# Performance work log

Measured on AMD Instinct MI355X. Metric: run time of the kernel, lower is better.

## Reference

```python
import jax, jax.numpy as jnp
import numpy as np

NEG = -1e6  # mask value used by d2l-style masked_softmax


def masked_softmax(scores, valid_lens):
    # scores: [B, Q, K]; valid_lens: [B] int — mask key positions j >= valid_len
    K = scores.shape[-1]
    mask = jnp.arange(K, dtype=jnp.int32)[None, None, :] < valid_lens[:, None, None]
    scores = jnp.where(mask, scores, NEG)
    return jax.nn.softmax(scores, axis=-1)


def setup_inputs() -> dict:
    key = jax.random.key(0)
    kq, kk, kv, kl = jax.random.split(key, 4)
    B, Q, K, d = 16, 4096, 4096, 128
    queries = jax.random.normal(kq, (B, Q, d), dtype=jnp.float32)
    keys = jax.random.normal(kk, (B, K, d), dtype=jnp.float32)
    values = jax.random.normal(kv, (B, K, d), dtype=jnp.float32)
    valid_lens = jax.random.randint(kl, (B,), 1, K + 1, dtype=jnp.int32)
    return {"queries": queries, "keys": keys, "values": values,
            "valid_lens": valid_lens}


def reference(queries, keys, values, valid_lens):
    d = queries.shape[-1]
    # [B, Q, K] scores = Q K^T / sqrt(d)
    scores = jnp.einsum('bqd,bkd->bqk', queries, keys) / jnp.sqrt(
        jnp.asarray(d, queries.dtype))
    attn = masked_softmax(scores, valid_lens)
    # dropout is identity in eval mode
    return jnp.einsum('bqk,bkd->bqd', attn, values)
```

## Files before the change

kernel.cpp:

```cpp
#include <hip/hip_runtime.h>
#include <stdint.h>

typedef __attribute__((ext_vector_type(8))) short short8;
typedef __attribute__((ext_vector_type(4))) float float4v;
typedef __attribute__((ext_vector_type(16))) float f32x16;

#define B_  16
#define S_  4096
#define D_  128
#define TM  64
#define TN  64
#define NT_ (S_ / TN)
#define IMG 8192

#define ZERO16 {0.f,0.f,0.f,0.f, 0.f,0.f,0.f,0.f, 0.f,0.f,0.f,0.f, 0.f,0.f,0.f,0.f}

__device__ __forceinline__ unsigned short f2bf(float f) {
    union { float f; uint32_t u; } c; c.f = f;
    uint32_t u = c.u + 0x7FFFu + ((c.u >> 16) & 1u);
    return (unsigned short)(u >> 16);
}

__device__ __forceinline__ uint4 pack8(float4v x, float4v y) {
    uint4 r;
    r.x = (uint32_t)f2bf(x[0]) | ((uint32_t)f2bf(x[1]) << 16);
    r.y = (uint32_t)f2bf(x[2]) | ((uint32_t)f2bf(x[3]) << 16);
    r.z = (uint32_t)f2bf(y[0]) | ((uint32_t)f2bf(y[1]) << 16);
    r.w = (uint32_t)f2bf(y[2]) | ((uint32_t)f2bf(y[3]) << 16);
    return r;
}

__device__ __forceinline__ void gload16(const unsigned short* g, unsigned short* l) {
    __builtin_amdgcn_global_load_lds(
        (const __attribute__((address_space(1))) unsigned int*)g,
        (__attribute__((address_space(3))) unsigned int*)l, 16, 0, 0);
}

__device__ __forceinline__ uint32_t cvtpk(float lo, float hi) {
    uint32_t w;
    asm("v_cvt_pk_bf16_f32 %0, %1, %2" : "=v"(w) : "v"(lo), "v"(hi));
    return w;
}

__device__ __forceinline__ short8 build_pfrag(const float* p) {
    uint32_t xa = cvtpk(p[0], p[1]);
    uint32_t xb = cvtpk(p[2], p[3]);
    uint32_t ya = cvtpk(p[4], p[5]);
    uint32_t yb = cvtpk(p[6], p[7]);
    asm("v_permlane32_swap_b32 %0, %1" : "+v"(xa), "+v"(ya));
    asm("v_permlane32_swap_b32 %0, %1" : "+v"(xb), "+v"(yb));
    union { uint32_t u[4]; short8 s; } r;
    r.u[0] = xa; r.u[1] = xb; r.u[2] = ya; r.u[3] = yb;
    return r.s;
}

__global__ __launch_bounds__(256)
void prepass(const float* __restrict__ Kg, const float* __restrict__ Vg,
             unsigned short* __restrict__ Kb, unsigned short* __restrict__ Vb)
{
    const int t = threadIdx.x;
    const int tile = blockIdx.x, b = blockIdx.y;
    const size_t img = (size_t)(b * NT_ + tile) * IMG;

    const float* ksrc = Kg + ((size_t)b * S_ + tile * TN) * D_;
    const float* vsrc = Vg + ((size_t)b * S_ + tile * TN) * D_;
    unsigned short* kdst = Kb + img;
    unsigned short* vdst = Vb + img;

    float4v kx[4], ky[4];
    #pragma unroll
    for (int i = 0; i < 4; ++i) {
        int bid = i * 256 + t;
        int row = bid >> 4, cbp = bid & 15;
        int cb  = cbp ^ (row & 15);
        const float* s = ksrc + row * D_ + cb * 8;
        kx[i] = *(const float4v*)s;
        ky[i] = *(const float4v*)(s + 4);
    }
    const int kb = t >> 5, cg = t & 31;
    float4v v[8];
    #pragma unroll
    for (int r = 0; r < 8; ++r)
        v[r] = *(const float4v*)(vsrc + (kb * 8 + r) * D_ + cg * 4);

    #pragma unroll
    for (int i = 0; i < 4; ++i) {
        int bid = i * 256 + t;
        *(uint4*)(kdst + (size_t)bid * 8) = pack8(kx[i], ky[i]);
    }

    #pragma unroll
    for (int j = 0; j < 4; ++j) {
        int dr = cg * 4 + j;
        uint4 w;
        w.x = (uint32_t)f2bf(v[0][j]) | ((uint32_t)f2bf(v[1][j]) << 16);
        w.y = (uint32_t)f2bf(v[2][j]) | ((uint32_t)f2bf(v[3][j]) << 16);
        w.z = (uint32_t)f2bf(v[4][j]) | ((uint32_t)f2bf(v[5][j]) << 16);
        w.w = (uint32_t)f2bf(v[6][j]) | ((uint32_t)f2bf(v[7][j]) << 16);
        *(uint4*)(vdst + dr * 64 + (kb ^ (dr & 7)) * 8) = w;
    }
}

__global__ __launch_bounds__(128, 2)
void attn_fwd(const float* __restrict__ Qg,
              const unsigned short* __restrict__ Kb,
              const unsigned short* __restrict__ Vb,
              const int* __restrict__ VL,
              float* __restrict__ Og)
{
    __shared__ __align__(16) unsigned short Ks[TN * D_];
    __shared__ __align__(16) unsigned short Vt[D_ * TN];

    const int t    = threadIdx.x;
    const int wave = t >> 6;
    const int lane = t & 63;
    const int l31  = lane & 31;
    const int hi   = lane >> 5;

    const int b  = blockIdx.y;
    const int q0 = blockIdx.x * TM;
    const int nvalid = VL[b];
    const int ntiles = (nvalid + TN - 1) / TN;

    const float qscale = 0.08838834764831845f * 1.4426950408889634f;

    short8 qf[8];
    {
        const float* qp = Qg + ((size_t)b * S_ + (q0 + wave * 32 + l31)) * D_;
        #pragma unroll
        for (int ks = 0; ks < 8; ++ks) {
            float4v x = *(const float4v*)(qp + ks * 16 + hi * 8);
            float4v y = *(const float4v*)(qp + ks * 16 + hi * 8 + 4);
            #pragma unroll
            for (int j = 0; j < 4; ++j) { x[j] *= qscale; y[j] *= qscale; }
            union { uint4 u; short8 s; } cv; cv.u = pack8(x, y);
            qf[ks] = cv.s;
        }
    }

    f32x16 zz = ZERO16;
    f32x16 oacc[4];
    oacc[0] = zz; oacc[1] = zz; oacc[2] = zz; oacc[3] = zz;
    float lsum = 0.f;

    const int swk = l31 & 15;
    const int swv = l31 & 7;

    for (int tile = 0; tile < ntiles; ++tile) {
        const int n0 = tile * TN;
        __syncthreads();

        {
            const unsigned short* kimg = Kb + (size_t)(b * NT_ + tile) * IMG;
            const unsigned short* vimg = Vb + (size_t)(b * NT_ + tile) * IMG;
            #pragma unroll
            for (int i = 0; i < 8; ++i) {
                int go = (i * 128 + t) * 8;
                int lo = (i * 128 + wave * 64) * 8;
                gload16(kimg + go, &Ks[lo]);
                gload16(vimg + go, &Vt[lo]);
            }
        }
        __syncthreads();

        f32x16 st0 = zz, st1 = zz;
        {
            const unsigned short* k0 = &Ks[l31 * D_];
            const unsigned short* k1 = &Ks[(32 + l31) * D_];
            __builtin_amdgcn_s_setprio(1);
            #pragma unroll
            for (int ks = 0; ks < 8; ++ks) {
                int sl = (((ks << 1) | hi) ^ swk) << 3;
                short8 a0 = *(const short8*)(k0 + sl);
                short8 a1 = *(const short8*)(k1 + sl);
                st0 = __builtin_amdgcn_mfma_f32_32x32x16_bf16(a0, qf[ks], st0, 0, 0, 0);
                st1 = __builtin_amdgcn_mfma_f32_32x32x16_bf16(a1, qf[ks], st1, 0, 0, 0);
            }
            __builtin_amdgcn_s_setprio(0);
        }

        float p0[16], p1[16];
        const bool full = (n0 + TN) <= nvalid;
        if (full) {
            #pragma unroll
            for (int r = 0; r < 16; ++r) { p0[r] = exp2f(st0[r]); lsum += p0[r]; }
            #pragma unroll
            for (int r = 0; r < 16; ++r) { p1[r] = exp2f(st1[r]); lsum += p1[r]; }
        } else {
            #pragma unroll
            for (int r = 0; r < 16; ++r) {
                int key = n0 + (r & 3) + 8 * (r >> 2) + 4 * hi;
                float e = exp2f(st0[r]);
                p0[r] = (key < nvalid) ? e : 0.f; lsum += p0[r];
            }
            #pragma unroll
            for (int r = 0; r < 16; ++r) {
                int key = n0 + 32 + (r & 3) + 8 * (r >> 2) + 4 * hi;
                float e = exp2f(st1[r]);
                p1[r] = (key < nvalid) ? e : 0.f; lsum += p1[r];
            }
        }

        short8 pf0 = build_pfrag(p0);
        short8 pf1 = build_pfrag(p0 + 8);
        short8 pf2 = build_pfrag(p1);
        short8 pf3 = build_pfrag(p1 + 8);

        __builtin_amdgcn_s_setprio(1);
        #pragma unroll
        for (int dt = 0; dt < 4; ++dt) {
            const unsigned short* vrow = &Vt[(dt * 32 + l31) * TN];
            short8 v0 = *(const short8*)(vrow + ((((0 << 1) | hi) ^ swv) << 3));
            short8 v1 = *(const short8*)(vrow + ((((1 << 1) | hi) ^ swv) << 3));
            short8 v2 = *(const short8*)(vrow + ((((2 << 1) | hi) ^ swv) << 3));
            short8 v3 = *(const short8*)(vrow + ((((3 << 1) | hi) ^ swv) << 3));
            oacc[dt] = __builtin_amdgcn_mfma_f32_32x32x16_bf16(pf0, v0, oacc[dt], 0, 0, 0);
            oacc[dt] = __builtin_amdgcn_mfma_f32_32x32x16_bf16(pf1, v1, oacc[dt], 0, 0, 0);
            oacc[dt] = __builtin_amdgcn_mfma_f32_32x32x16_bf16(pf2, v2, oacc[dt], 0, 0, 0);
            oacc[dt] = __builtin_amdgcn_mfma_f32_32x32x16_bf16(pf3, v3, oacc[dt], 0, 0, 0);
        }
        __builtin_amdgcn_s_setprio(0);
    }

    float ltot = lsum + __shfl_xor(lsum, 32);
    float inv  = 1.0f / ltot;

    float* op = Og + ((size_t)b * S_ + (q0 + wave * 32)) * D_ + l31;
    #pragma unroll
    for (int r = 0; r < 16; ++r) {
        const int qc = (r & 3) + 8 * (r >> 2);
        float invr = __shfl(inv, qc + 4 * hi, 32);
        #pragma unroll
        for (int dt = 0; dt < 4; ++dt)
            op[(qc + 4 * hi) * D_ + dt * 32] = oacc[dt][r] * invr;
    }
}

extern "C" void kernel_launch(void* const* d_in, const int* in_sizes, int n_in,
                              void* d_out, int out_size, void* d_ws, size_t ws_size,
                              hipStream_t stream) {
    const float* Q = (const float*)d_in[0];
    const float* K = (const float*)d_in[1];
    const float* V = (const float*)d_in[2];
    const int*   L = (const int*)d_in[3];
    float*       O = (float*)d_out;

    unsigned short* Kb = (unsigned short*)d_ws;
    unsigned short* Vb = Kb + (size_t)B_ * S_ * D_;

    dim3 grid(NT_, B_);
    prepass<<<grid, 256, 0, stream>>>(K, V, Kb, Vb);
    dim3 grid2(S_ / TM, B_);
    attn_fwd<<<grid2, 128, 0, stream>>>(Q, Kb, Vb, L, O);
}
```

Baseline: 240.2 us.

## Split key tile across two wave pairs and reduce partial outputs in shared memory

Doubles the block to four waves. Each pair of waves still covers the same 32 query rows, but each wave handles only half of the 64 keys in a tile, so per-wave MFMA work and register pressure are halved. Partial output accumulators and row sums from the second key half are reduced through shared memory at the end. The aim is more waves in flight to hide latency, at the cost of an extra LDS reduction, more barriers, and an occupancy target of four blocks in launch bounds.

```diff
diff --git a/kernel.cpp b/kernel.cpp
--- a/kernel.cpp
+++ b/kernel.cpp
@@ -101,21 +101,25 @@
     }
 }
 
-__global__ __launch_bounds__(128, 2)
+__global__ __launch_bounds__(256, 4)
 void attn_fwd(const float* __restrict__ Qg,
               const unsigned short* __restrict__ Kb,
               const unsigned short* __restrict__ Vb,
               const int* __restrict__ VL,
               float* __restrict__ Og)
 {
-    __shared__ __align__(16) unsigned short Ks[TN * D_];
-    __shared__ __align__(16) unsigned short Vt[D_ * TN];
+    __shared__ __align__(16) unsigned short SM[2 * IMG];
+    __shared__ float Ls[128];
+    unsigned short* Ks = SM;
+    unsigned short* Vt = SM + IMG;
 
     const int t    = threadIdx.x;
     const int wave = t >> 6;
     const int lane = t & 63;
     const int l31  = lane & 31;
     const int hi   = lane >> 5;
+    const int wq   = wave >> 1;
+    const int wk   = wave & 1;
 
     const int b  = blockIdx.y;
     const int q0 = blockIdx.x * TM;
@@ -126,7 +130,7 @@
 
     short8 qf[8];
     {
-        const float* qp = Qg + ((size_t)b * S_ + (q0 + wave * 32 + l31)) * D_;
+        const float* qp = Qg + ((size_t)b * S_ + (q0 + wq * 32 + l31)) * D_;
         #pragma unroll
         for (int ks = 0; ks < 8; ++ks) {
             float4v x = *(const float4v*)(qp + ks * 16 + hi * 8);
@@ -154,85 +158,91 @@
             const unsigned short* kimg = Kb + (size_t)(b * NT_ + tile) * IMG;
             const unsigned short* vimg = Vb + (size_t)(b * NT_ + tile) * IMG;
             #pragma unroll
-            for (int i = 0; i < 8; ++i) {
-                int go = (i * 128 + t) * 8;
-                int lo = (i * 128 + wave * 64) * 8;
+            for (int i = 0; i < 4; ++i) {
+                int go = (i * 256 + t) * 8;
+                int lo = (i * 256 + wave * 64) * 8;
                 gload16(kimg + go, &Ks[lo]);
                 gload16(vimg + go, &Vt[lo]);
             }
         }
         __syncthreads();
 
-        f32x16 st0 = zz, st1 = zz;
+        f32x16 st = zz;
         {
-            const unsigned short* k0 = &Ks[l31 * D_];
-            const unsigned short* k1 = &Ks[(32 + l31) * D_];
+            const unsigned short* k0 = &Ks[(wk * 32 + l31) * D_];
             __builtin_amdgcn_s_setprio(1);
             #pragma unroll
             for (int ks = 0; ks < 8; ++ks) {
                 int sl = (((ks << 1) | hi) ^ swk) << 3;
                 short8 a0 = *(const short8*)(k0 + sl);
-                short8 a1 = *(const short8*)(k1 + sl);
-                st0 = __builtin_amdgcn_mfma_f32_32x32x16_bf16(a0, qf[ks], st0, 0, 0, 0);
-                st1 = __builtin_amdgcn_mfma_f32_32x32x16_bf16(a1, qf[ks], st1, 0, 0, 0);
+                st = __builtin_amdgcn_mfma_f32_32x32x16_bf16(a0, qf[ks], st, 0, 0, 0);
             }
             __builtin_amdgcn_s_setprio(0);
         }
 
-        float p0[16], p1[16];
+        float p[16];
         const bool full = (n0 + TN) <= nvalid;
         if (full) {
             #pragma unroll
-            for (int r = 0; r < 16; ++r) { p0[r] = exp2f(st0[r]); lsum += p0[r]; }
-            #pragma unroll
-            for (int r = 0; r < 16; ++r) { p1[r] = exp2f(st1[r]); lsum += p1[r]; }
+            for (int r = 0; r < 16; ++r) { p[r] = exp2f(st[r]); lsum += p[r]; }
         } else {
             #pragma unroll
             for (int r = 0; r < 16; ++r) {
-                int key = n0 + (r & 3) + 8 * (r >> 2) + 4 * hi;
-                float e = exp2f(st0[r]);
-                p0[r] = (key < nvalid) ? e : 0.f; lsum += p0[r];
+                int key = n0 + wk * 32 + (r & 3) + 8 * (r >> 2) + 4 * hi;
+                float e = exp2f(st[r]);
+                p[r] = (key < nvalid) ? e : 0.f; lsum += p[r];
             }
-            #pragma unroll
-            for (int r = 0; r < 16; ++r) {
-                int key = n0 + 32 + (r & 3) + 8 * (r >> 2) + 4 * hi;
-                float e = exp2f(st1[r]);
-                p1[r] = (key < nvalid) ? e : 0.f; lsum += p1[r];
-            }
-        }
-
-        short8 pf0 = build_pfrag(p0);
-        short8 pf1 = build_pfrag(p0 + 8);
-        short8 pf2 = build_pfrag(p1);
-        short8 pf3 = build_pfrag(p1 + 8);
+        }
+
+        short8 pf0 = build_pfrag(p);
+        short8 pf1 = build_pfrag(p + 8);
 
         __builtin_amdgcn_s_setprio(1);
         #pragma unroll
         for (int dt = 0; dt < 4; ++dt) {
             const unsigned short* vrow = &Vt[(dt * 32 + l31) * TN];
-            short8 v0 = *(const short8*)(vrow + ((((0 << 1) | hi) ^ swv) << 3));
-            short8 v1 = *(const short8*)(vrow + ((((1 << 1) | hi) ^ swv) << 3));
-            short8 v2 = *(const short8*)(vrow + ((((2 << 1) | hi) ^ swv) << 3));
-            short8 v3 = *(const short8*)(vrow + ((((3 << 1) | hi) ^ swv) << 3));
+            int s0 = ((((wk * 2 + 0) << 1) | hi) ^ swv) << 3;
+            int s1 = ((((wk * 2 + 1) << 1) | hi) ^ swv) << 3;
+            short8 v0 = *(const short8*)(vrow + s0);
+            short8 v1 = *(const short8*)(vrow + s1);
             oacc[dt] = __builtin_amdgcn_mfma_f32_32x32x16_bf16(pf0, v0, oacc[dt], 0, 0, 0);
             oacc[dt] = __builtin_amdgcn_mfma_f32_32x32x16_bf16(pf1, v1, oacc[dt], 0, 0, 0);
-            oacc[dt] = __builtin_amdgcn_mfma_f32_32x32x16_bf16(pf2, v2, oacc[dt], 0, 0, 0);
-            oacc[dt] = __builtin_amdgcn_mfma_f32_32x32x16_bf16(pf3, v3, oacc[dt], 0, 0, 0);
         }
         __builtin_amdgcn_s_setprio(0);
     }
 
-    float ltot = lsum + __shfl_xor(lsum, 32);
-    float inv  = 1.0f / ltot;
-
-    float* op = Og + ((size_t)b * S_ + (q0 + wave * 32)) * D_ + l31;
-    #pragma unroll
-    for (int r = 0; r < 16; ++r) {
-        const int qc = (r & 3) + 8 * (r >> 2);
-        float invr = __shfl(inv, qc + 4 * hi, 32);
+    float lpart = lsum + __shfl_xor(lsum, 32);
+
+    float* red = (float*)SM;
+    __syncthreads();
+    if (wk == 1) {
         #pragma unroll
         for (int dt = 0; dt < 4; ++dt)
-            op[(qc + 4 * hi) * D_ + dt * 32] = oacc[dt][r] * invr;
+            #pragma unroll
+            for (int r = 0; r < 16; ++r)
+                red[(dt * 16 + r) * 128 + wq * 64 + lane] = oacc[dt][r];
+        Ls[wq * 64 + lane] = lpart;
+    }
+    __syncthreads();
+    if (wk == 0) {
+        #pragma unroll
+        for (int dt = 0; dt < 4; ++dt)
+            #pragma unroll
+            for (int r = 0; r < 16; ++r)
+                oacc[dt][r] += red[(dt * 16 + r) * 128 + wq * 64 + lane];
+
+        float ltot = lpart + Ls[wq * 64 + lane];
+        float inv  = 1.0f / ltot;
+
+        float* op = Og + ((size_t)b * S_ + (q0 + wq * 32)) * D_ + l31;
+        #pragma unroll
+        for (int r = 0; r < 16; ++r) {
+            const int qc = (r & 3) + 8 * (r >> 2);
+            float invr = __shfl(inv, qc + 4 * hi, 32);
+            #pragma unroll
+            for (int dt = 0; dt < 4; ++dt)
+                op[(qc + 4 * hi) * D_ + dt * 32] = oacc[dt][r] * invr;
+        }
     }
 }
 
@@ -251,5 +261,5 @@
     dim3 grid(NT_, B_);
     prepass<<<grid, 256, 0, stream>>>(K, V, Kb, Vb);
     dim3 grid2(S_ / TM, B_);
-    attn_fwd<<<grid2, 128, 0, stream>>>(Q, Kb, Vb, L, O);
-}
+    attn_fwd<<<grid2, 256, 0, stream>>>(Q, Kb, Vb, L, O);
+}
```

Measured after the change: 275.1 us. +14.5%, slower.
